# Optimization experiments

Hardware: AMD Instinct MI355X
Metric: run time of the kernel (lower is better)

## Reference

```python
import jax, jax.numpy as jnp
import numpy as np

B, S, I, H, O = 1024, 512, 64, 128, 1  # batch, seq_len, input_size, hidden_size, output_size


def setup_inputs() -> dict:
    key = jax.random.key(0)
    ks = jax.random.split(key, 8)
    def w(k, shape, fan):
        return jax.random.normal(k, shape, jnp.float32) * (1.0 / np.sqrt(fan))
    return {
        "x":    jax.random.normal(ks[0], (B, S, I), jnp.float32),
        # feas0: Linear(I, 4I)
        "W0":   w(ks[1], (4 * I, I), I),
        "b0":   jnp.zeros((4 * I,), jnp.float32),
        # feas: Linear(4I, I)
        "W1":   w(ks[2], (I, 4 * I), 4 * I),
        "b1":   jnp.zeros((I,), jnp.float32),
        # LSTM (PyTorch gate order i, f, g, o)
        "W_ih": w(ks[3], (4 * H, I), H),
        "W_hh": w(ks[4], (4 * H, H), H),
        "b_ih": jnp.zeros((4 * H,), jnp.float32),
        "b_hh": jnp.zeros((4 * H,), jnp.float32),
        # fc_h2finaloutput: Linear(H, O)
        "Wf":   w(ks[5], (O, H), H),
        "bf":   jnp.zeros((O,), jnp.float32),
    }


def reference(x, W0, b0, W1, b1, W_ih, W_hh, b_ih, b_hh, Wf, bf):
    # feas(feas0(x)); dropout is identity in eval mode
    h = jnp.einsum("bsi,ji->bsj", x, W0) + b0          # [B,S,4I]
    r = jnp.einsum("bsj,ij->bsi", h, W1) + b1          # [B,S,I]
    xr = jax.nn.relu(r + x)                             # residual + ReLU

    # Precompute input-side gate projections once: [S,B,4H] (scan over time)
    xg = jnp.einsum("bsi,gi->sbg", xr, W_ih) + b_ih + b_hh

    def step(carry, g_x):
        hprev, cprev = carry
        g = g_x + hprev @ W_hh.T                        # [B,4H]
        i, f, gg, o = jnp.split(g, 4, axis=-1)
        c = jax.nn.sigmoid(f) * cprev + jax.nn.sigmoid(i) * jnp.tanh(gg)
        hn = jax.nn.sigmoid(o) * jnp.tanh(c)
        return (hn, c), None

    z = jnp.zeros((x.shape[0], W_hh.shape[1]), x.dtype)
    (hT, _), _ = jax.lax.scan(step, (z, z), xg)         # only last h is needed

    out = hT @ Wf.T + bf                                # [B,O]
    return out.reshape(out.shape[0] * out.shape[1], -1) # view(B*O, -1)
```

## Files before the change

### kernel.cpp

```cpp
#include <hip/hip_runtime.h>
#include <stdint.h>
#include <stddef.h>

#define B_ 1024
#define S_ 512
#define I_ 64
#define H_ 128
#define G_ 512
#define KTOT 192
#define ROWS 4
#define RSTRIDE 288
#define HBUF (ROWS * RSTRIDE)
#define XRSTRIDE 160
#define XRBUF (ROWS * XRSTRIDE)

typedef __bf16 bf16;
typedef __bf16 bf16x8 __attribute__((ext_vector_type(8)));
typedef float f32x4 __attribute__((ext_vector_type(4)));
typedef unsigned short u16;
typedef unsigned short u16x4 __attribute__((ext_vector_type(4)));

#define WS_WCT  ((size_t)0)
#define WS_BIAS (WS_WCT + (size_t)G_*KTOT*2)
#define WS_M16  (WS_BIAS + (size_t)G_*4)
#define WS_CVEC (WS_M16 + (size_t)I_*I_*2)

__global__ __launch_bounds__(256) void precompute_kernel(
    const float* __restrict__ W0, const float* __restrict__ b0,
    const float* __restrict__ W1, const float* __restrict__ b1,
    const float* __restrict__ W_ih, const float* __restrict__ W_hh,
    const float* __restrict__ b_ih, const float* __restrict__ b_hh,
    char* __restrict__ ws)
{
  int tid = blockIdx.x * 256 + threadIdx.x;
  bf16*  m16     = (bf16*)(ws + WS_M16);
  float* cvec    = (float*)(ws + WS_CVEC);
  float* biascat = (float*)(ws + WS_BIAS);
  bf16*  wct     = (bf16*)(ws + WS_WCT);

  if (tid < 4096) {
    int i = tid >> 6, k = tid & 63;
    float acc = 0.f;
    for (int j = 0; j < 256; ++j) acc += W1[i*256 + j] * W0[j*64 + k];
    m16[tid] = (bf16)acc;
  } else if (tid < 4160) {
    int i = tid - 4096;
    float acc = b1[i];
    for (int j = 0; j < 256; ++j) acc += W1[i*256 + j] * b0[j];
    cvec[i] = acc;
  } else if (tid < 4672) {
    int n = tid - 4160;
    biascat[n] = b_ih[n] + b_hh[n];
  }
  for (int e = tid; e < G_*KTOT; e += 16384) {
    int n = e / KTOT, k = e % KTOT;
    float v = (k < I_) ? W_ih[n*I_ + k] : W_hh[n*H_ + (k - I_)];
    wct[e] = (bf16)v;
  }
}

__device__ inline float sigmf(float x) {
  float e = __builtin_amdgcn_exp2f(-1.4426950408889634f * x);
  return __builtin_amdgcn_rcpf(1.f + e);
}
__device__ inline float tanhf_(float x) {
  float e = __builtin_amdgcn_exp2f(-2.8853900817779268f * x);
  float r = __builtin_amdgcn_rcpf(1.f + e);
  return 2.f * r - 1.f;
}

__global__ __launch_bounds__(512, 2) void scan_kernel(
    const char* __restrict__ ws, const float* __restrict__ x,
    const float* __restrict__ Wf, const float* __restrict__ bfp,
    float* __restrict__ out)
{
  const bf16*  __restrict__ wct     = (const bf16*)(ws + WS_WCT);
  const float* __restrict__ biascat = (const float*)(ws + WS_BIAS);
  const bf16*  __restrict__ m16     = (const bf16*)(ws + WS_M16);
  const float* __restrict__ cvec    = (const float*)(ws + WS_CVEC);

  __shared__ __align__(16) char h_lds[2 * HBUF];
  __shared__ __align__(16) char xr_lds[2 * XRBUF];
  __shared__ __align__(16) float stageG[8][4][16][4];

  const int tid = threadIdx.x;
  const int w  = tid >> 6;
  const int l  = tid & 63;
  const int lr = l & 15;
  const int lg = l >> 4;
  const int ar = lr & (ROWS - 1);
  const int wm = w & 3;
  const int b0 = blockIdx.x * ROWS;

  for (int t = tid; t < HBUF/4; t += 512) reinterpret_cast<int*>(h_lds)[t] = 0;

  bf16x8 wfrag[4][6];
  #pragma unroll
  for (int q = 0; q < 4; ++q) {
    int n = q*128 + w*16 + lr;
    #pragma unroll
    for (int kc = 0; kc < 6; ++kc)
      wfrag[q][kc] = *reinterpret_cast<const bf16x8*>(wct + n*KTOT + kc*32 + lg*8);
  }
  float bias[4];
  #pragma unroll
  for (int q = 0; q < 4; ++q) bias[q] = biascat[q*128 + w*16 + lr];

  bf16x8 mfrag[2];
  #pragma unroll
  for (int kc = 0; kc < 2; ++kc)
    mfrag[kc] = *reinterpret_cast<const bf16x8*>(m16 + (wm*16 + lr)*64 + kc*32 + lg*8);
  f32x4 cvec4 = *reinterpret_cast<const f32x4*>(cvec + wm*16 + lg*4);

  f32x4 xq0, xq1, xq2, xq3, xres;
  const size_t xrow = ((size_t)(b0 + ar) * S_) * I_;
  if (w < 4) {
    const float* bx = x + xrow + 0*I_;
    xq0 = *reinterpret_cast<const f32x4*>(bx + lg*8);
    xq1 = *reinterpret_cast<const f32x4*>(bx + lg*8 + 4);
    xq2 = *reinterpret_cast<const f32x4*>(bx + 32 + lg*8);
    xq3 = *reinterpret_cast<const f32x4*>(bx + 32 + lg*8 + 4);
    xres = *reinterpret_cast<const f32x4*>(bx + wm*16 + lg*4);

    bf16x8 xf0, xf1;
    #pragma unroll
    for (int j = 0; j < 4; ++j) {
      xf0[j] = (bf16)xq0[j]; xf0[4+j] = (bf16)xq1[j];
      xf1[j] = (bf16)xq2[j]; xf1[4+j] = (bf16)xq3[j];
    }
    f32x4 fa = {0.f, 0.f, 0.f, 0.f};
    fa = __builtin_amdgcn_mfma_f32_16x16x32_bf16(mfrag[0], xf0, fa, 0, 0, 0);
    fa = __builtin_amdgcn_mfma_f32_16x16x32_bf16(mfrag[1], xf1, fa, 0, 0, 0);
    if (lr < ROWS) {
      u16x4 pk;
      #pragma unroll
      for (int r = 0; r < 4; ++r) {
        float t = fa[r] + cvec4[r] + xres[r];
        t = t > 0.f ? t : 0.f;
        pk[r] = __builtin_bit_cast(u16, (bf16)t);
      }
      *reinterpret_cast<u16x4*>(xr_lds + lr*XRSTRIDE + (wm*16 + lg*4)*2) = pk;
    }
    const float* b1x = x + xrow + 1*I_;
    xq0 = *reinterpret_cast<const f32x4*>(b1x + lg*8);
    xq1 = *reinterpret_cast<const f32x4*>(b1x + lg*8 + 4);
    xq2 = *reinterpret_cast<const f32x4*>(b1x + 32 + lg*8);
    xq3 = *reinterpret_cast<const f32x4*>(b1x + 32 + lg*8 + 4);
    xres = *reinterpret_cast<const f32x4*>(b1x + wm*16 + lg*4);
  }

  float c1 = 0.f;
  __syncthreads();

  for (int s = 0; s < S_; ++s) {
    f32x4 nq0, nq1, nq2, nq3, nres;
    if (w < 4) {
      int sn2 = (s + 2 < S_) ? s + 2 : S_ - 1;
      const float* bx = x + xrow + (size_t)sn2 * I_;
      nq0 = *reinterpret_cast<const f32x4*>(bx + lg*8);
      nq1 = *reinterpret_cast<const f32x4*>(bx + lg*8 + 4);
      nq2 = *reinterpret_cast<const f32x4*>(bx + 32 + lg*8);
      nq3 = *reinterpret_cast<const f32x4*>(bx + 32 + lg*8 + 4);
      nres = *reinterpret_cast<const f32x4*>(bx + wm*16 + lg*4);
    }

    const char* rbh = h_lds  + ((s & 1) ? HBUF  : 0);
    char*       wbh = h_lds  + ((s & 1) ? 0     : HBUF);
    const char* rbx = xr_lds + ((s & 1) ? XRBUF : 0);
    char*       wbx = xr_lds + ((s & 1) ? 0     : XRBUF);

    bf16x8 axr[2], ah[4];
    #pragma unroll
    for (int kc = 0; kc < 2; ++kc)
      axr[kc] = *reinterpret_cast<const bf16x8*>(rbx + ar*XRSTRIDE + kc*64 + lg*16);
    #pragma unroll
    for (int kc = 0; kc < 4; ++kc)
      ah[kc] = *reinterpret_cast<const bf16x8*>(rbh + ar*RSTRIDE + kc*64 + lg*16);

    f32x4 acc[4];
    #pragma unroll
    for (int q = 0; q < 4; ++q) {
      acc[q] = (f32x4){bias[q], bias[q], bias[q], bias[q]};
      acc[q] = __builtin_amdgcn_mfma_f32_16x16x32_bf16(axr[0], wfrag[q][0], acc[q], 0, 0, 0);
      acc[q] = __builtin_amdgcn_mfma_f32_16x16x32_bf16(axr[1], wfrag[q][1], acc[q], 0, 0, 0);
      #pragma unroll
      for (int kc = 0; kc < 4; ++kc)
        acc[q] = __builtin_amdgcn_mfma_f32_16x16x32_bf16(ah[kc], wfrag[q][2+kc], acc[q], 0, 0, 0);
    }

    if (w < 4) {
      bf16x8 xf0, xf1;
      #pragma unroll
      for (int j = 0; j < 4; ++j) {
        xf0[j] = (bf16)xq0[j]; xf0[4+j] = (bf16)xq1[j];
        xf1[j] = (bf16)xq2[j]; xf1[4+j] = (bf16)xq3[j];
      }
      f32x4 fa = {0.f, 0.f, 0.f, 0.f};
      fa = __builtin_amdgcn_mfma_f32_16x16x32_bf16(mfrag[0], xf0, fa, 0, 0, 0);
      fa = __builtin_amdgcn_mfma_f32_16x16x32_bf16(mfrag[1], xf1, fa, 0, 0, 0);
      if (lr < ROWS) {
        u16x4 pk;
        #pragma unroll
        for (int r = 0; r < 4; ++r) {
          float t = fa[r] + cvec4[r] + xres[r];
          t = t > 0.f ? t : 0.f;
          pk[r] = __builtin_bit_cast(u16, (bf16)t);
        }
        *reinterpret_cast<u16x4*>(wbx + lr*XRSTRIDE + (wm*16 + lg*4)*2) = pk;
      }
    }

    if (l < 16) {
      #pragma unroll
      for (int q = 0; q < 4; ++q)
        *reinterpret_cast<f32x4*>(&stageG[w][q][l][0]) = acc[q];
    }
    float g4[4];
    #pragma unroll
    for (int q = 0; q < 4; ++q) g4[q] = stageG[w][q][lr][lg];

    float ii = sigmf(g4[0]);
    float ff = sigmf(g4[1]);
    float gg = tanhf_(g4[2]);
    float oo = sigmf(g4[3]);
    float cn = ff * c1 + ii * gg;
    c1 = cn;
    float hn = oo * tanhf_(cn);
    *reinterpret_cast<bf16*>(wbh + lg*RSTRIDE + (w*16 + lr)*2) = (bf16)hn;

    __syncthreads();
    if (w < 4) { xq0=nq0; xq1=nq1; xq2=nq2; xq3=nq3; xres=nres; }
  }

  if (tid < 64) {
    int row = lg, cl = lr * 8;
    bf16x8 hv = *reinterpret_cast<const bf16x8*>(h_lds + row*RSTRIDE + cl*2);
    float accf = 0.f;
    #pragma unroll
    for (int j = 0; j < 8; ++j) accf += (float)hv[j] * Wf[cl + j];
    accf += __shfl_xor(accf, 1, 64);
    accf += __shfl_xor(accf, 2, 64);
    accf += __shfl_xor(accf, 4, 64);
    accf += __shfl_xor(accf, 8, 64);
    if (lr == 0) out[b0 + row] = accf + bfp[0];
  }
}

extern "C" void kernel_launch(void* const* d_in, const int* in_sizes, int n_in,
                              void* d_out, int out_size, void* d_ws, size_t ws_size,
                              hipStream_t stream)
{
  const float* x    = (const float*)d_in[0];
  const float* W0   = (const float*)d_in[1];
  const float* b0   = (const float*)d_in[2];
  const float* W1   = (const float*)d_in[3];
  const float* b1   = (const float*)d_in[4];
  const float* W_ih = (const float*)d_in[5];
  const float* W_hh = (const float*)d_in[6];
  const float* b_ih = (const float*)d_in[7];
  const float* b_hh = (const float*)d_in[8];
  const float* Wf   = (const float*)d_in[9];
  const float* bf   = (const float*)d_in[10];
  char* ws = (char*)d_ws;
  float* out = (float*)d_out;

  hipLaunchKernelGGL(precompute_kernel, dim3(64), dim3(256), 0, stream,
                     W0, b0, W1, b1, W_ih, W_hh, b_ih, b_hh, ws);
  hipLaunchKernelGGL(scan_kernel, dim3(256), dim3(512), 0, stream,
                     ws, x, Wf, bf, out);
}
```

Before: 611.4 us.

## Drop LDS gate staging, unroll scan by two, and relax per-step barrier

Removes the stageG shared-memory round trip by having each lane pick its gate value directly from the MFMA accumulator. This works because the A-operand rows repeat with period four, so accumulator element lg holds batch row lg. The time loop is unrolled by two so the double-buffer offsets become constants. The x prefetch now runs two independent register sets to hide global-load latency across steps. The per-step barrier waits only on LDS traffic, so outstanding global loads stay in flight, and it is fenced with sched_barrier. The cost is more registers and a hand-written synchronisation sequence that depends on the loads being consumed correctly.

```diff
diff --git a/kernel.cpp b/kernel.cpp
--- a/kernel.cpp
+++ b/kernel.cpp
@@ -69,6 +69,77 @@
   return 2.f * r - 1.f;
 }
 
+#define SELQ(A) ((lg & 2) ? ((lg & 1) ? (A)[3] : (A)[2]) \
+                          : ((lg & 1) ? (A)[1] : (A)[0]))
+
+#define LSTM_STEP(P, XQ0, XQ1, XQ2, XQ3, XRES, SN)                            \
+  {                                                                           \
+          \
+    bf16x8 axr0 = *(const bf16x8*)(xr_rd + (P)*XRBUF);                        \
+    bf16x8 axr1 = *(const bf16x8*)(xr_rd + (P)*XRBUF + 64);                   \
+    bf16x8 ah0  = *(const bf16x8*)(h_rd + (P)*HBUF);                          \
+    bf16x8 ah1  = *(const bf16x8*)(h_rd + (P)*HBUF + 64);                     \
+    bf16x8 ah2  = *(const bf16x8*)(h_rd + (P)*HBUF + 128);                    \
+    bf16x8 ah3  = *(const bf16x8*)(h_rd + (P)*HBUF + 192);                    \
+          \
+    f32x4 fa = {0.f, 0.f, 0.f, 0.f};                                          \
+    if (w < 4) {                                                              \
+      bf16x8 xf0, xf1;                                                        \
+      _Pragma("unroll")                                                       \
+      for (int j = 0; j < 4; ++j) {                                           \
+        xf0[j] = (bf16)XQ0[j]; xf0[4+j] = (bf16)XQ1[j];                       \
+        xf1[j] = (bf16)XQ2[j]; xf1[4+j] = (bf16)XQ3[j];                       \
+      }                                                                       \
+      fa = __builtin_amdgcn_mfma_f32_16x16x32_bf16(mfrag0, xf0, fa, 0,0,0);   \
+      fa = __builtin_amdgcn_mfma_f32_16x16x32_bf16(mfrag1, xf1, fa, 0,0,0);   \
+    }                                                                         \
+                  \
+    f32x4 acc[4];                                                             \
+    _Pragma("unroll")                                                         \
+    for (int q = 0; q < 4; ++q) {                                             \
+      acc[q] = (f32x4){0.f, 0.f, 0.f, 0.f};                                   \
+      acc[q] = __builtin_amdgcn_mfma_f32_16x16x32_bf16(axr0, wfrag[q][0], acc[q], 0,0,0); \
+      acc[q] = __builtin_amdgcn_mfma_f32_16x16x32_bf16(axr1, wfrag[q][1], acc[q], 0,0,0); \
+      acc[q] = __builtin_amdgcn_mfma_f32_16x16x32_bf16(ah0,  wfrag[q][2], acc[q], 0,0,0); \
+      acc[q] = __builtin_amdgcn_mfma_f32_16x16x32_bf16(ah1,  wfrag[q][3], acc[q], 0,0,0); \
+      acc[q] = __builtin_amdgcn_mfma_f32_16x16x32_bf16(ah2,  wfrag[q][4], acc[q], 0,0,0); \
+      acc[q] = __builtin_amdgcn_mfma_f32_16x16x32_bf16(ah3,  wfrag[q][5], acc[q], 0,0,0); \
+    }                                                                         \
+       \
+    float ii = sigmf(SELQ(acc[0]) + bias[0]);                                 \
+    float ff = sigmf(SELQ(acc[1]) + bias[1]);                                 \
+    float gg = tanhf_(SELQ(acc[2]) + bias[2]);                                \
+    float oo = sigmf(SELQ(acc[3]) + bias[3]);                                 \
+    float cn = ff * c1 + ii * gg;                                             \
+    c1 = cn;                                                                  \
+    float hn = oo * tanhf_(cn);                                               \
+    *(bf16*)(h_wr + ((P)^1)*HBUF) = (bf16)hn;                                 \
+    if (w < 4) {                                                              \
+      if (lr < ROWS) {               \
+        u16x4 pk;                                                             \
+        _Pragma("unroll")                                                     \
+        for (int r = 0; r < 4; ++r) {                                         \
+          float t = fa[r] + cvec4[r] + XRES[r];                               \
+          t = t > 0.f ? t : 0.f;                                              \
+          pk[r] = __builtin_bit_cast(u16, (bf16)t);                           \
+        }                                                                     \
+        *(u16x4*)(xr_wr + ((P)^1)*XRBUF) = pk;                                \
+      }                                                                       \
+            \
+      const float* bx = x + xrow + (size_t)(SN) * I_;                         \
+      XQ0 = *(const f32x4*)(bx + lg*8);                                       \
+      XQ1 = *(const f32x4*)(bx + lg*8 + 4);                                   \
+      XQ2 = *(const f32x4*)(bx + 32 + lg*8);                                  \
+      XQ3 = *(const f32x4*)(bx + 32 + lg*8 + 4);                              \
+      XRES = *(const f32x4*)(bx + w*16 + lg*4);                               \
+    }                                                                         \
+                \
+    __builtin_amdgcn_sched_barrier(0);                                        \
+    asm volatile("s_waitcnt lgkmcnt(0)" ::: "memory");                        \
+    __builtin_amdgcn_s_barrier();                                             \
+    __builtin_amdgcn_sched_barrier(0);                                        \
+  }
+
 __global__ __launch_bounds__(512, 2) void scan_kernel(
     const char* __restrict__ ws, const float* __restrict__ x,
     const float* __restrict__ Wf, const float* __restrict__ bfp,
@@ -81,7 +152,6 @@
 
   __shared__ __align__(16) char h_lds[2 * HBUF];
   __shared__ __align__(16) char xr_lds[2 * XRBUF];
-  __shared__ __align__(16) float stageG[8][4][16][4];
 
   const int tid = threadIdx.x;
   const int w  = tid >> 6;
@@ -89,10 +159,12 @@
   const int lr = l & 15;
   const int lg = l >> 4;
   const int ar = lr & (ROWS - 1);
-  const int wm = w & 3;
   const int b0 = blockIdx.x * ROWS;
 
-  for (int t = tid; t < HBUF/4; t += 512) reinterpret_cast<int*>(h_lds)[t] = 0;
+  char* xr_rd = xr_lds + ar*XRSTRIDE + lg*16;
+  char* h_rd  = h_lds  + ar*RSTRIDE  + lg*16;
+  char* h_wr  = h_lds  + lg*RSTRIDE  + (w*16 + lr)*2;
+  char* xr_wr = xr_lds + lr*XRSTRIDE + (w*16 + lg*4)*2;
 
   bf16x8 wfrag[4][6];
   #pragma unroll
@@ -106,130 +178,64 @@
   #pragma unroll
   for (int q = 0; q < 4; ++q) bias[q] = biascat[q*128 + w*16 + lr];
 
-  bf16x8 mfrag[2];
-  #pragma unroll
-  for (int kc = 0; kc < 2; ++kc)
-    mfrag[kc] = *reinterpret_cast<const bf16x8*>(m16 + (wm*16 + lr)*64 + kc*32 + lg*8);
-  f32x4 cvec4 = *reinterpret_cast<const f32x4*>(cvec + wm*16 + lg*4);
-
-  f32x4 xq0, xq1, xq2, xq3, xres;
-  const size_t xrow = ((size_t)(b0 + ar) * S_) * I_;
+  bf16x8 mfrag0 = *reinterpret_cast<const bf16x8*>(m16 + ((w&3)*16 + lr)*64 + lg*8);
+  bf16x8 mfrag1 = *reinterpret_cast<const bf16x8*>(m16 + ((w&3)*16 + lr)*64 + 32 + lg*8);
+  f32x4 cvec4 = *reinterpret_cast<const f32x4*>(cvec + (w&3)*16 + lg*4);
+
+  for (int t = tid; t < HBUF/4; t += 512) reinterpret_cast<int*>(h_lds)[t] = 0;
+
+  const size_t xrow = (size_t)(b0 + ar) * S_ * I_;
+  f32x4 aq0={0,0,0,0}, aq1={0,0,0,0}, aq2={0,0,0,0}, aq3={0,0,0,0}, ares={0,0,0,0};
+  f32x4 bq0={0,0,0,0}, bq1={0,0,0,0}, bq2={0,0,0,0}, bq3={0,0,0,0}, bres={0,0,0,0};
   if (w < 4) {
-    const float* bx = x + xrow + 0*I_;
-    xq0 = *reinterpret_cast<const f32x4*>(bx + lg*8);
-    xq1 = *reinterpret_cast<const f32x4*>(bx + lg*8 + 4);
-    xq2 = *reinterpret_cast<const f32x4*>(bx + 32 + lg*8);
-    xq3 = *reinterpret_cast<const f32x4*>(bx + 32 + lg*8 + 4);
-    xres = *reinterpret_cast<const f32x4*>(bx + wm*16 + lg*4);
-
+    const float* bx = x + xrow;
+    f32x4 q0 = *(const f32x4*)(bx + lg*8);
+    f32x4 q1 = *(const f32x4*)(bx + lg*8 + 4);
+    f32x4 q2 = *(const f32x4*)(bx + 32 + lg*8);
+    f32x4 q3 = *(const f32x4*)(bx + 32 + lg*8 + 4);
+    f32x4 rs = *(const f32x4*)(bx + w*16 + lg*4);
     bf16x8 xf0, xf1;
     #pragma unroll
     for (int j = 0; j < 4; ++j) {
-      xf0[j] = (bf16)xq0[j]; xf0[4+j] = (bf16)xq1[j];
-      xf1[j] = (bf16)xq2[j]; xf1[4+j] = (bf16)xq3[j];
+      xf0[j] = (bf16)q0[j]; xf0[4+j] = (bf16)q1[j];
+      xf1[j] = (bf16)q2[j]; xf1[4+j] = (bf16)q3[j];
     }
     f32x4 fa = {0.f, 0.f, 0.f, 0.f};
-    fa = __builtin_amdgcn_mfma_f32_16x16x32_bf16(mfrag[0], xf0, fa, 0, 0, 0);
-    fa = __builtin_amdgcn_mfma_f32_16x16x32_bf16(mfrag[1], xf1, fa, 0, 0, 0);
+    fa = __builtin_amdgcn_mfma_f32_16x16x32_bf16(mfrag0, xf0, fa, 0, 0, 0);
+    fa = __builtin_amdgcn_mfma_f32_16x16x32_bf16(mfrag1, xf1, fa, 0, 0, 0);
     if (lr < ROWS) {
       u16x4 pk;
       #pragma unroll
       for (int r = 0; r < 4; ++r) {
-        float t = fa[r] + cvec4[r] + xres[r];
+        float t = fa[r] + cvec4[r] + rs[r];
         t = t > 0.f ? t : 0.f;
         pk[r] = __builtin_bit_cast(u16, (bf16)t);
       }
-      *reinterpret_cast<u16x4*>(xr_lds + lr*XRSTRIDE + (wm*16 + lg*4)*2) = pk;
+      *(u16x4*)(xr_wr) = pk;
     }
-    const float* b1x = x + xrow + 1*I_;
-    xq0 = *reinterpret_cast<const f32x4*>(b1x + lg*8);
-    xq1 = *reinterpret_cast<const f32x4*>(b1x + lg*8 + 4);
-    xq2 = *reinterpret_cast<const f32x4*>(b1x + 32 + lg*8);
-    xq3 = *reinterpret_cast<const f32x4*>(b1x + 32 + lg*8 + 4);
-    xres = *reinterpret_cast<const f32x4*>(b1x + wm*16 + lg*4);
+    const float* bx1 = x + xrow + I_;
+    aq0 = *(const f32x4*)(bx1 + lg*8);
+    aq1 = *(const f32x4*)(bx1 + lg*8 + 4);
+    aq2 = *(const f32x4*)(bx1 + 32 + lg*8);
+    aq3 = *(const f32x4*)(bx1 + 32 + lg*8 + 4);
+    ares = *(const f32x4*)(bx1 + w*16 + lg*4);
+    const float* bx2 = x + xrow + 2*I_;
+    bq0 = *(const f32x4*)(bx2 + lg*8);
+    bq1 = *(const f32x4*)(bx2 + lg*8 + 4);
+    bq2 = *(const f32x4*)(bx2 + 32 + lg*8);
+    bq3 = *(const f32x4*)(bx2 + 32 + lg*8 + 4);
+    bres = *(const f32x4*)(bx2 + w*16 + lg*4);
   }
 
   float c1 = 0.f;
   __syncthreads();
 
-  for (int s = 0; s < S_; ++s) {
-    f32x4 nq0, nq1, nq2, nq3, nres;
-    if (w < 4) {
-      int sn2 = (s + 2 < S_) ? s + 2 : S_ - 1;
-      const float* bx = x + xrow + (size_t)sn2 * I_;
-      nq0 = *reinterpret_cast<const f32x4*>(bx + lg*8);
-      nq1 = *reinterpret_cast<const f32x4*>(bx + lg*8 + 4);
-      nq2 = *reinterpret_cast<const f32x4*>(bx + 32 + lg*8);
-      nq3 = *reinterpret_cast<const f32x4*>(bx + 32 + lg*8 + 4);
-      nres = *reinterpret_cast<const f32x4*>(bx + wm*16 + lg*4);
-    }
-
-    const char* rbh = h_lds  + ((s & 1) ? HBUF  : 0);
-    char*       wbh = h_lds  + ((s & 1) ? 0     : HBUF);
-    const char* rbx = xr_lds + ((s & 1) ? XRBUF : 0);
-    char*       wbx = xr_lds + ((s & 1) ? 0     : XRBUF);
-
-    bf16x8 axr[2], ah[4];
-    #pragma unroll
-    for (int kc = 0; kc < 2; ++kc)
-      axr[kc] = *reinterpret_cast<const bf16x8*>(rbx + ar*XRSTRIDE + kc*64 + lg*16);
-    #pragma unroll
-    for (int kc = 0; kc < 4; ++kc)
-      ah[kc] = *reinterpret_cast<const bf16x8*>(rbh + ar*RSTRIDE + kc*64 + lg*16);
-
-    f32x4 acc[4];
-    #pragma unroll
-    for (int q = 0; q < 4; ++q) {
-      acc[q] = (f32x4){bias[q], bias[q], bias[q], bias[q]};
-      acc[q] = __builtin_amdgcn_mfma_f32_16x16x32_bf16(axr[0], wfrag[q][0], acc[q], 0, 0, 0);
-      acc[q] = __builtin_amdgcn_mfma_f32_16x16x32_bf16(axr[1], wfrag[q][1], acc[q], 0, 0, 0);
-      #pragma unroll
-      for (int kc = 0; kc < 4; ++kc)
-        acc[q] = __builtin_amdgcn_mfma_f32_16x16x32_bf16(ah[kc], wfrag[q][2+kc], acc[q], 0, 0, 0);
-    }
-
-    if (w < 4) {
-      bf16x8 xf0, xf1;
-      #pragma unroll
-      for (int j = 0; j < 4; ++j) {
-        xf0[j] = (bf16)xq0[j]; xf0[4+j] = (bf16)xq1[j];
-        xf1[j] = (bf16)xq2[j]; xf1[4+j] = (bf16)xq3[j];
-      }
-      f32x4 fa = {0.f, 0.f, 0.f, 0.f};
-      fa = __builtin_amdgcn_mfma_f32_16x16x32_bf16(mfrag[0], xf0, fa, 0, 0, 0);
-      fa = __builtin_amdgcn_mfma_f32_16x16x32_bf16(mfrag[1], xf1, fa, 0, 0, 0);
-      if (lr < ROWS) {
-        u16x4 pk;
-        #pragma unroll
-        for (int r = 0; r < 4; ++r) {
-          float t = fa[r] + cvec4[r] + xres[r];
-          t = t > 0.f ? t : 0.f;
-          pk[r] = __builtin_bit_cast(u16, (bf16)t);
-        }
-        *reinterpret_cast<u16x4*>(wbx + lr*XRSTRIDE + (wm*16 + lg*4)*2) = pk;
-      }
-    }
-
-    if (l < 16) {
-      #pragma unroll
-      for (int q = 0; q < 4; ++q)
-        *reinterpret_cast<f32x4*>(&stageG[w][q][l][0]) = acc[q];
-    }
-    float g4[4];
-    #pragma unroll
-    for (int q = 0; q < 4; ++q) g4[q] = stageG[w][q][lr][lg];
-
-    float ii = sigmf(g4[0]);
-    float ff = sigmf(g4[1]);
-    float gg = tanhf_(g4[2]);
-    float oo = sigmf(g4[3]);
-    float cn = ff * c1 + ii * gg;
-    c1 = cn;
-    float hn = oo * tanhf_(cn);
-    *reinterpret_cast<bf16*>(wbh + lg*RSTRIDE + (w*16 + lr)*2) = (bf16)hn;
-
-    __syncthreads();
-    if (w < 4) { xq0=nq0; xq1=nq1; xq2=nq2; xq3=nq3; xres=nres; }
+  for (int it = 0; it < S_/2; ++it) {
+    int s0 = 2*it;
+    int sn3 = (s0 + 3 < S_) ? s0 + 3 : S_ - 1;
+    int sn4 = (s0 + 4 < S_) ? s0 + 4 : S_ - 1;
+    LSTM_STEP(0, aq0, aq1, aq2, aq3, ares, sn3)
+    LSTM_STEP(1, bq0, bq1, bq2, bq3, bres, sn4)
   }
 
   if (tid < 64) {
```

Measured after the change: 665.6 us. 8.9% more time.
